# Kernel tuning notes

Hardware: AMD Instinct MI355X
Metric: run time of the kernel (lower is better)

## Reference

```python
import jax, jax.numpy as jnp
import numpy as np

B = 32768          # batch (replay-buffer minibatch)
OBS, ACT = 17, 6   # HalfCheetah-style dims
IN = OBS + ACT
H = 256            # hidden width hard-coded in the module
N = 10             # num_q_nets


def setup_inputs() -> dict:
    key = jax.random.key(0)
    ks = jax.random.split(key, 8)
    # PyTorch Linear default init: U(-1/sqrt(fan_in), 1/sqrt(fan_in)); scale randn similarly.
    s1, s2, s3 = 1.0 / np.sqrt(IN), 1.0 / np.sqrt(H), 1.0 / np.sqrt(H)
    return {
        "state": jax.random.normal(ks[0], (B, OBS), dtype=jnp.float32),
        "action": jax.random.uniform(ks[1], (B, ACT), dtype=jnp.float32, minval=-1.0, maxval=1.0),
        "W1": jax.random.normal(ks[2], (N, IN, H), dtype=jnp.float32) * s1,
        "b1": jax.random.normal(ks[3], (N, H), dtype=jnp.float32) * s1,
        "W2": jax.random.normal(ks[4], (N, H, H), dtype=jnp.float32) * s2,
        "b2": jax.random.normal(ks[5], (N, H), dtype=jnp.float32) * s2,
        "W3": jax.random.normal(ks[6], (N, H, 1), dtype=jnp.float32) * s3,
        "b3": jax.random.normal(ks[7], (N, 1), dtype=jnp.float32) * s3,
    }


def reference(state, action, W1, b1, W2, b2, W3, b3):
    # x: [B, OBS+ACT]
    x = jnp.concatenate([state, action], axis=1)
    # batched-over-ensemble GEMMs; n=ensemble member, b=batch
    h1 = jax.nn.relu(jnp.einsum("bi,nih->nbh", x, W1) + b1[:, None, :])   # [N,B,H]
    h2 = jax.nn.relu(jnp.einsum("nbh,nho->nbo", h1, W2) + b2[:, None, :])  # [N,B,H]
    out = jnp.einsum("nbh,nho->nbo", h2, W3) + b3[:, None, :]              # [N,B,1]
    return out
```

## Files before the change

### kernel.cpp

```cpp
#include <hip/hip_runtime.h>
#include <hip/hip_bf16.h>


typedef __attribute__((ext_vector_type(8))) short bf16x8;
typedef __attribute__((ext_vector_type(4))) float f32x4;

#define B_TOTAL 32768
#define NQ 10
#define HDIM 256
#define BT 128

#define XP_ELEMS  (B_TOTAL * 32)
#define W1P_ELEMS (NQ * 16 * 64 * 8)
#define W2P_ELEMS (NQ * 8 * 16 * 64 * 8)

__device__ __forceinline__ unsigned short f2bf(float f) {
  unsigned int u = __float_as_uint(f);
  u = u + 0x7FFFu + ((u >> 16) & 1u);
  return (unsigned short)(u >> 16);
}

__device__ __forceinline__ unsigned int pk2bf(float a, float b) {
  union { __hip_bfloat162 h; unsigned int u; } cv;
  cv.h = __float22bfloat162_rn(make_float2(a, b));
  return cv.u;
}

__global__ void pack_all_kernel(const float* __restrict__ state,
                                const float* __restrict__ action,
                                const float* __restrict__ W1,
                                const float* __restrict__ W2,
                                unsigned short* __restrict__ xp,
                                unsigned short* __restrict__ w1p,
                                unsigned short* __restrict__ w2p) {
  int t = blockIdx.x * 256 + threadIdx.x;
  const int NX  = B_TOTAL * 4;
  const int NW1 = NQ * 16 * 64;
  if (t < NX) {
    int b = t >> 2, seg = t & 3;
    unsigned short v[8];
    if (seg < 2) {
      const float* sp = state + (size_t)b * 17 + seg * 8;
#pragma unroll
      for (int j = 0; j < 8; j++) v[j] = f2bf(sp[j]);
    } else if (seg == 2) {
      v[0] = f2bf(state[(size_t)b * 17 + 16]);
#pragma unroll
      for (int j = 0; j < 6; j++) v[1 + j] = f2bf(action[(size_t)b * 6 + j]);
      v[7] = 0;
    } else {
#pragma unroll
      for (int j = 0; j < 8; j++) v[j] = 0;
    }
    *(uint4*)&xp[(size_t)t * 8] = *(const uint4*)v;
  } else if (t < NX + NW1) {
    int u = t - NX;
    int lane = u & 63, mt = (u >> 6) & 15, n = u >> 10;
    int m = lane & 15, q = lane >> 4;
    int outc = mt * 16 + m;
    unsigned short v[8];
#pragma unroll
    for (int j = 0; j < 8; j++) {
      int k = q * 8 + j;
      v[j] = (k < 23) ? f2bf(W1[(n * 23 + k) * 256 + outc]) : (unsigned short)0;
    }
    *(uint4*)&w1p[(size_t)u * 8] = *(const uint4*)v;
  } else {
    int u = t - NX - NW1;
    int lane = u & 63, mt = (u >> 6) & 15, kt = (u >> 10) & 7, n = u >> 13;
    int m = lane & 15, q = lane >> 4;
    int outc = mt * 16 + m;
    unsigned short v[8];
#pragma unroll
    for (int j = 0; j < 8; j++) {
      int h = kt * 32 + q * 8 + j;
      v[j] = f2bf(W2[((size_t)(n * 256 + h)) * 256 + outc]);
    }
    *(uint4*)&w2p[(size_t)u * 8] = *(const uint4*)v;
  }
}

__global__ __launch_bounds__(512, 4) void fused_ensemble_kernel(
    const unsigned short* __restrict__ xp,
    const unsigned short* __restrict__ w1p,
    const float* __restrict__ b1,
    const unsigned short* __restrict__ w2p,
    const float* __restrict__ b2,
    const float* __restrict__ W3,
    const float* __restrict__ b3,
    float* __restrict__ out) {
  __shared__ __align__(16) unsigned short hs[32 * BT * 8];
  __shared__ float red[8 * 64];

  const int tid = threadIdx.x;
  const int lane = tid & 63;
  const int w = tid >> 6;
  const int m = lane & 15;
  const int q = lane >> 4;
  const int cg = w >> 1;
  const int colg = w & 1;

  const int n = blockIdx.x >> 8;
  const int row0 = (blockIdx.x & 255) * BT;

  const unsigned short* w2n = w2p + (size_t)n * (8 * 16 * 64 * 8);

  f32x4 acc[4][4];
  {
    bf16x8 af[4], bfr[4];
#pragma unroll
    for (int nt = 0; nt < 4; nt++) {
      int col = row0 + colg * 64 + nt * 16 + m;
      bfr[nt] = *(const bf16x8*)(xp + (size_t)col * 32 + q * 8);
    }
#pragma unroll
    for (int mt = 0; mt < 4; mt++)
      af[mt] = *(const bf16x8*)(w1p + (((size_t)n * 16 + cg * 4 + mt) * 64 + lane) * 8);
#pragma unroll
    for (int mt = 0; mt < 4; mt++) {
      float4 bv = *(const float4*)&b1[n * HDIM + (cg * 4 + mt) * 16 + q * 4];
      f32x4 bi = (f32x4){bv.x, bv.y, bv.z, bv.w};
#pragma unroll
      for (int nt = 0; nt < 4; nt++) acc[mt][nt] = bi;
    }
#pragma unroll
    for (int nt = 0; nt < 4; nt++)
#pragma unroll
      for (int mt = 0; mt < 4; mt++)
        acc[mt][nt] = __builtin_amdgcn_mfma_f32_16x16x32_bf16(af[mt], bfr[nt], acc[mt][nt], 0, 0, 0);
  }

  bf16x8 aS[2][4];
  bf16x8 bS[2][4];
#pragma unroll
  for (int sl = 0; sl < 2; sl++)
#pragma unroll
    for (int mt = 0; mt < 4; mt++)
      aS[sl][mt] = *(const bf16x8*)(w2n + (((size_t)sl * 16 + cg * 4 + mt) * 64 + lane) * 8);

  f32x4 acc2[4][4];
#pragma unroll
  for (int mt = 0; mt < 4; mt++) {
    float4 bv = *(const float4*)&b2[n * HDIM + (cg * 4 + mt) * 16 + q * 4];
    f32x4 bi = (f32x4){bv.x, bv.y, bv.z, bv.w};
#pragma unroll
    for (int nt = 0; nt < 4; nt++) acc2[mt][nt] = bi;
  }

#pragma unroll
  for (int mt = 0; mt < 4; mt++) {
    int kq = cg * 8 + mt * 2 + (q >> 1);
    int joff = (q & 1) * 4;
#pragma unroll
    for (int nt = 0; nt < 4; nt++) {
      int col = colg * 64 + nt * 16 + m;
      f32x4 a = acc[mt][nt];
      uint2 wv;
      wv.x = pk2bf(fmaxf(a[0], 0.f), fmaxf(a[1], 0.f));
      wv.y = pk2bf(fmaxf(a[2], 0.f), fmaxf(a[3], 0.f));
      *(uint2*)&hs[((size_t)kq * BT + col) * 8 + joff] = wv;
    }
  }
  __syncthreads();

  {
#pragma unroll
    for (int sl = 0; sl < 2; sl++)
#pragma unroll
      for (int nt = 0; nt < 4; nt++)
        bS[sl][nt] = *(const bf16x8*)&hs[(((size_t)sl * 4 + q) * BT + colg * 64 + nt * 16 + m) * 8];

#pragma unroll
    for (int kt = 0; kt < 8; kt++) {
      const int sl = kt & 1;
#pragma unroll
      for (int nt = 0; nt < 4; nt++)
#pragma unroll
        for (int mt = 0; mt < 4; mt++)
          acc2[mt][nt] = __builtin_amdgcn_mfma_f32_16x16x32_bf16(
              aS[sl][mt], bS[sl][nt], acc2[mt][nt], 0, 0, 0);
      if (kt + 2 < 8) {
#pragma unroll
        for (int mt = 0; mt < 4; mt++)
          aS[sl][mt] = *(const bf16x8*)(w2n + (((size_t)(kt + 2) * 16 + cg * 4 + mt) * 64 + lane) * 8);
#pragma unroll
        for (int nt = 0; nt < 4; nt++)
          bS[sl][nt] = *(const bf16x8*)&hs[(((size_t)(kt + 2) * 4 + q) * BT + colg * 64 + nt * 16 + m) * 8];
      }
    }
  }

  {
    float4 w3v[4];
#pragma unroll
    for (int mt = 0; mt < 4; mt++)
      w3v[mt] = *(const float4*)&W3[n * HDIM + (cg * 4 + mt) * 16 + q * 4];
    float p[4];
#pragma unroll
    for (int nt = 0; nt < 4; nt++) {
      float s = 0.f;
#pragma unroll
      for (int mt = 0; mt < 4; mt++) {
        f32x4 a = acc2[mt][nt];
        float4 wv = w3v[mt];
        s = fmaf(fmaxf(a[0], 0.f), wv.x, s);
        s = fmaf(fmaxf(a[1], 0.f), wv.y, s);
        s = fmaf(fmaxf(a[2], 0.f), wv.z, s);
        s = fmaf(fmaxf(a[3], 0.f), wv.w, s);
      }
      s += __shfl_xor(s, 16, 64);
      s += __shfl_xor(s, 32, 64);
      p[nt] = s;
    }
    if (q == 0) {
#pragma unroll
      for (int nt = 0; nt < 4; nt++) red[w * 64 + nt * 16 + m] = p[nt];
    }
    __syncthreads();
    if (tid < BT) {
      int g = tid >> 6, lc = tid & 63;
      float s = b3[n];
#pragma unroll
      for (int c = 0; c < 4; c++) s += red[(c * 2 + g) * 64 + lc];
      out[(size_t)n * B_TOTAL + row0 + tid] = s;
    }
  }
}

extern "C" void kernel_launch(void* const* d_in, const int* in_sizes, int n_in,
                              void* d_out, int out_size, void* d_ws, size_t ws_size,
                              hipStream_t stream) {
  const float* state  = (const float*)d_in[0];
  const float* action = (const float*)d_in[1];
  const float* W1 = (const float*)d_in[2];
  const float* b1 = (const float*)d_in[3];
  const float* W2 = (const float*)d_in[4];
  const float* b2 = (const float*)d_in[5];
  const float* W3 = (const float*)d_in[6];
  const float* b3 = (const float*)d_in[7];
  float* out = (float*)d_out;

  unsigned short* xp  = (unsigned short*)d_ws;
  unsigned short* w1p = (unsigned short*)((char*)d_ws + (size_t)XP_ELEMS * 2);
  unsigned short* w2p = (unsigned short*)((char*)d_ws + (size_t)(XP_ELEMS + W1P_ELEMS) * 2);

  pack_all_kernel<<<872, 256, 0, stream>>>(state, action, W1, W2, xp, w1p, w2p);
  fused_ensemble_kernel<<<NQ * (B_TOTAL / BT), 512, 0, stream>>>(
      xp, w1p, b1, w2p, b2, W3, b3, out);
}
```

Measured before the change: 120.6 us.

## Replace block barrier with per-pair LDS flags and rotated K-loop order

The workgroup-wide barrier between layer-1 output staging and the layer-2 GEMM is replaced by per-column-group atomic counters in shared memory. Each wave first consumes the K-slices its own pair of waves produced, then the others in rotated order, spinning with s_sleep until the producing pair has signalled. This is meant to let waves start layer-2 MFMAs without waiting for the whole block. It adds an extra barrier at kernel start, spin-wait and atomic overhead, and changes how the W2 and hidden-state loads are prefetched.

```diff
diff --git a/kernel.cpp b/kernel.cpp
--- a/kernel.cpp
+++ b/kernel.cpp
@@ -91,6 +91,7 @@
     float* __restrict__ out) {
   __shared__ __align__(16) unsigned short hs[32 * BT * 8];
   __shared__ float red[8 * 64];
+  __shared__ int flg[4];
 
   const int tid = threadIdx.x;
   const int lane = tid & 63;
@@ -105,6 +106,9 @@
 
   const unsigned short* w2n = w2p + (size_t)n * (8 * 16 * 64 * 8);
 
+  if (tid < 4) flg[tid] = 0;
+  __syncthreads();
+
   f32x4 acc[4][4];
   {
     bf16x8 af[4], bfr[4];
@@ -130,13 +134,11 @@
         acc[mt][nt] = __builtin_amdgcn_mfma_f32_16x16x32_bf16(af[mt], bfr[nt], acc[mt][nt], 0, 0, 0);
   }
 
-  bf16x8 aS[2][4];
-  bf16x8 bS[2][4];
-#pragma unroll
-  for (int sl = 0; sl < 2; sl++)
-#pragma unroll
-    for (int mt = 0; mt < 4; mt++)
-      aS[sl][mt] = *(const bf16x8*)(w2n + (((size_t)sl * 16 + cg * 4 + mt) * 64 + lane) * 8);
+  bf16x8 aE[4];
+  const int kt0 = 2 * cg;
+#pragma unroll
+  for (int mt = 0; mt < 4; mt++)
+    aE[mt] = *(const bf16x8*)(w2n + (((size_t)kt0 * 16 + cg * 4 + mt) * 64 + lane) * 8);
 
   f32x4 acc2[4][4];
 #pragma unroll
@@ -161,32 +163,44 @@
       *(uint2*)&hs[((size_t)kq * BT + col) * 8 + joff] = wv;
     }
   }
-  __syncthreads();
+  __threadfence_block();
+  if (lane == 0)
+    __hip_atomic_fetch_add(&flg[cg], 1, __ATOMIC_RELEASE, __HIP_MEMORY_SCOPE_WORKGROUP);
 
   {
 #pragma unroll
-    for (int sl = 0; sl < 2; sl++)
-#pragma unroll
-      for (int nt = 0; nt < 4; nt++)
-        bS[sl][nt] = *(const bf16x8*)&hs[(((size_t)sl * 4 + q) * BT + colg * 64 + nt * 16 + m) * 8];
-
-#pragma unroll
-    for (int kt = 0; kt < 8; kt++) {
-      const int sl = kt & 1;
+    for (int ii = 0; ii < 4; ii++) {
+      const int ktE = (2 * cg + 2 * ii) & 7;
+      const int pair = ktE >> 1;
+      while (__hip_atomic_load(&flg[pair], __ATOMIC_ACQUIRE, __HIP_MEMORY_SCOPE_WORKGROUP) < 2) {
+        __builtin_amdgcn_s_sleep(1);
+      }
+      bf16x8 bE[4], bO[4], aO[4];
+#pragma unroll
+      for (int nt = 0; nt < 4; nt++)
+        bE[nt] = *(const bf16x8*)&hs[(((size_t)ktE * 4 + q) * BT + colg * 64 + nt * 16 + m) * 8];
+#pragma unroll
+      for (int nt = 0; nt < 4; nt++)
+        bO[nt] = *(const bf16x8*)&hs[(((size_t)(ktE + 1) * 4 + q) * BT + colg * 64 + nt * 16 + m) * 8];
+#pragma unroll
+      for (int mt = 0; mt < 4; mt++)
+        aO[mt] = *(const bf16x8*)(w2n + (((size_t)(ktE + 1) * 16 + cg * 4 + mt) * 64 + lane) * 8);
 #pragma unroll
       for (int nt = 0; nt < 4; nt++)
 #pragma unroll
         for (int mt = 0; mt < 4; mt++)
-          acc2[mt][nt] = __builtin_amdgcn_mfma_f32_16x16x32_bf16(
-              aS[sl][mt], bS[sl][nt], acc2[mt][nt], 0, 0, 0);
-      if (kt + 2 < 8) {
+          acc2[mt][nt] = __builtin_amdgcn_mfma_f32_16x16x32_bf16(aE[mt], bE[nt], acc2[mt][nt], 0, 0, 0);
+      if (ii < 3) {
+        const int ktN = (ktE + 2) & 7;
 #pragma unroll
         for (int mt = 0; mt < 4; mt++)
-          aS[sl][mt] = *(const bf16x8*)(w2n + (((size_t)(kt + 2) * 16 + cg * 4 + mt) * 64 + lane) * 8);
-#pragma unroll
-        for (int nt = 0; nt < 4; nt++)
-          bS[sl][nt] = *(const bf16x8*)&hs[(((size_t)(kt + 2) * 4 + q) * BT + colg * 64 + nt * 16 + m) * 8];
+          aE[mt] = *(const bf16x8*)(w2n + (((size_t)ktN * 16 + cg * 4 + mt) * 64 + lane) * 8);
       }
+#pragma unroll
+      for (int nt = 0; nt < 4; nt++)
+#pragma unroll
+        for (int mt = 0; mt < 4; mt++)
+          acc2[mt][nt] = __builtin_amdgcn_mfma_f32_16x16x32_bf16(aO[mt], bO[nt], acc2[mt][nt], 0, 0, 0);
     }
   }
 
```

Result: slower. 125.9 us (+4.3%).

## Make ensemble MLP kernel persistent with W2 slice held in registers

Applied to the files above, without the earlier changes.

Turns the fused kernel into a persistent one: the grid is 52 blocks per ensemble member, each with 4 waves, and each block loops over 64-row batch tiles. Each wave loads its W2 slice for all K steps into registers once and reuses it for every tile, so W2 is no longer re-streamed from cache for every 128-row block. In exchange, each wave needs many more registers, blocks are smaller, fewer waves are resident per CU to hide latency, and 512 tiles do not split evenly across 52 blocks.

```diff
diff --git a/kernel.cpp b/kernel.cpp
--- a/kernel.cpp
+++ b/kernel.cpp
@@ -8,7 +8,9 @@
 #define B_TOTAL 32768
 #define NQ 10
 #define HDIM 256
-#define BT 128
+#define BT 64
+#define TILES 512
+#define BPN 52
 
 #define XP_ELEMS  (B_TOTAL * 32)
 #define W1P_ELEMS (NQ * 16 * 64 * 8)
@@ -80,7 +82,7 @@
   }
 }
 
-__global__ __launch_bounds__(512, 4) void fused_ensemble_kernel(
+__global__ __launch_bounds__(256, 2) void fused_ensemble_kernel(
     const unsigned short* __restrict__ xp,
     const unsigned short* __restrict__ w1p,
     const float* __restrict__ b1,
@@ -90,139 +92,139 @@
     const float* __restrict__ b3,
     float* __restrict__ out) {
   __shared__ __align__(16) unsigned short hs[32 * BT * 8];
-  __shared__ float red[8 * 64];
+  __shared__ float red[4 * BT];
 
   const int tid = threadIdx.x;
   const int lane = tid & 63;
   const int w = tid >> 6;
   const int m = lane & 15;
   const int q = lane >> 4;
-  const int cg = w >> 1;
-  const int colg = w & 1;
-
-  const int n = blockIdx.x >> 8;
-  const int row0 = (blockIdx.x & 255) * BT;
+
+  const int n = blockIdx.x / BPN;
+  const int slot = blockIdx.x - n * BPN;
 
   const unsigned short* w2n = w2p + (size_t)n * (8 * 16 * 64 * 8);
 
-  f32x4 acc[4][4];
-  {
-    bf16x8 af[4], bfr[4];
-#pragma unroll
-    for (int nt = 0; nt < 4; nt++) {
-      int col = row0 + colg * 64 + nt * 16 + m;
-      bfr[nt] = *(const bf16x8*)(xp + (size_t)col * 32 + q * 8);
-    }
+  bf16x8 aW[8][4];
+#pragma unroll
+  for (int kt = 0; kt < 8; kt++)
 #pragma unroll
     for (int mt = 0; mt < 4; mt++)
-      af[mt] = *(const bf16x8*)(w1p + (((size_t)n * 16 + cg * 4 + mt) * 64 + lane) * 8);
+      aW[kt][mt] = *(const bf16x8*)(w2n + (((size_t)kt * 16 + w * 4 + mt) * 64 + lane) * 8);
+
+  const float b3n = b3[n];
+
+  for (int tile = slot; tile < TILES; tile += BPN) {
+    const int row0 = tile * BT;
+
+    f32x4 acc[4][4];
+    {
+      bf16x8 af[4], bfr[4];
+#pragma unroll
+      for (int nt = 0; nt < 4; nt++) {
+        int col = row0 + nt * 16 + m;
+        bfr[nt] = *(const bf16x8*)(xp + (size_t)col * 32 + q * 8);
+      }
+#pragma unroll
+      for (int mt = 0; mt < 4; mt++)
+        af[mt] = *(const bf16x8*)(w1p + (((size_t)n * 16 + w * 4 + mt) * 64 + lane) * 8);
+#pragma unroll
+      for (int mt = 0; mt < 4; mt++) {
+        float4 bv = *(const float4*)&b1[n * HDIM + (w * 4 + mt) * 16 + q * 4];
+        f32x4 bi = (f32x4){bv.x, bv.y, bv.z, bv.w};
+#pragma unroll
+        for (int nt = 0; nt < 4; nt++) acc[mt][nt] = bi;
+      }
+#pragma unroll
+      for (int nt = 0; nt < 4; nt++)
+#pragma unroll
+        for (int mt = 0; mt < 4; mt++)
+          acc[mt][nt] = __builtin_amdgcn_mfma_f32_16x16x32_bf16(af[mt], bfr[nt], acc[mt][nt], 0, 0, 0);
+    }
+
 #pragma unroll
     for (int mt = 0; mt < 4; mt++) {
-      float4 bv = *(const float4*)&b1[n * HDIM + (cg * 4 + mt) * 16 + q * 4];
+      int kq = w * 8 + mt * 2 + (q >> 1);
+      int joff = (q & 1) * 4;
+#pragma unroll
+      for (int nt = 0; nt < 4; nt++) {
+        int col = nt * 16 + m;
+        f32x4 a = acc[mt][nt];
+        uint2 wv;
+        wv.x = pk2bf(fmaxf(a[0], 0.f), fmaxf(a[1], 0.f));
+        wv.y = pk2bf(fmaxf(a[2], 0.f), fmaxf(a[3], 0.f));
+        *(uint2*)&hs[((size_t)kq * BT + col) * 8 + joff] = wv;
+      }
+    }
+
+    f32x4 acc2[4][4];
+#pragma unroll
+    for (int mt = 0; mt < 4; mt++) {
+      float4 bv = *(const float4*)&b2[n * HDIM + (w * 4 + mt) * 16 + q * 4];
       f32x4 bi = (f32x4){bv.x, bv.y, bv.z, bv.w};
 #pragma unroll
-      for (int nt = 0; nt < 4; nt++) acc[mt][nt] = bi;
-    }
-#pragma unroll
-    for (int nt = 0; nt < 4; nt++)
+      for (int nt = 0; nt < 4; nt++) acc2[mt][nt] = bi;
+    }
+    __syncthreads();
+
+    {
+      bf16x8 bS[2][4];
+#pragma unroll
+      for (int sl = 0; sl < 2; sl++)
+#pragma unroll
+        for (int nt = 0; nt < 4; nt++)
+          bS[sl][nt] = *(const bf16x8*)&hs[(((size_t)sl * 4 + q) * BT + nt * 16 + m) * 8];
+
+#pragma unroll
+      for (int kt = 0; kt < 8; kt++) {
+        const int sl = kt & 1;
+#pragma unroll
+        for (int nt = 0; nt < 4; nt++)
+#pragma unroll
+          for (int mt = 0; mt < 4; mt++)
+            acc2[mt][nt] = __builtin_amdgcn_mfma_f32_16x16x32_bf16(
+                aW[kt][mt], bS[sl][nt], acc2[mt][nt], 0, 0, 0);
+        if (kt + 2 < 8) {
+#pragma unroll
+          for (int nt = 0; nt < 4; nt++)
+            bS[sl][nt] = *(const bf16x8*)&hs[(((size_t)(kt + 2) * 4 + q) * BT + nt * 16 + m) * 8];
+        }
+      }
+    }
+
+    {
+      float4 w3v[4];
 #pragma unroll
       for (int mt = 0; mt < 4; mt++)
-        acc[mt][nt] = __builtin_amdgcn_mfma_f32_16x16x32_bf16(af[mt], bfr[nt], acc[mt][nt], 0, 0, 0);
-  }
-
-  bf16x8 aS[2][4];
-  bf16x8 bS[2][4];
-#pragma unroll
-  for (int sl = 0; sl < 2; sl++)
-#pragma unroll
-    for (int mt = 0; mt < 4; mt++)
-      aS[sl][mt] = *(const bf16x8*)(w2n + (((size_t)sl * 16 + cg * 4 + mt) * 64 + lane) * 8);
-
-  f32x4 acc2[4][4];
-#pragma unroll
-  for (int mt = 0; mt < 4; mt++) {
-    float4 bv = *(const float4*)&b2[n * HDIM + (cg * 4 + mt) * 16 + q * 4];
-    f32x4 bi = (f32x4){bv.x, bv.y, bv.z, bv.w};
-#pragma unroll
-    for (int nt = 0; nt < 4; nt++) acc2[mt][nt] = bi;
-  }
-
-#pragma unroll
-  for (int mt = 0; mt < 4; mt++) {
-    int kq = cg * 8 + mt * 2 + (q >> 1);
-    int joff = (q & 1) * 4;
-#pragma unroll
-    for (int nt = 0; nt < 4; nt++) {
-      int col = colg * 64 + nt * 16 + m;
-      f32x4 a = acc[mt][nt];
-      uint2 wv;
-      wv.x = pk2bf(fmaxf(a[0], 0.f), fmaxf(a[1], 0.f));
-      wv.y = pk2bf(fmaxf(a[2], 0.f), fmaxf(a[3], 0.f));
-      *(uint2*)&hs[((size_t)kq * BT + col) * 8 + joff] = wv;
-    }
-  }
-  __syncthreads();
-
-  {
-#pragma unroll
-    for (int sl = 0; sl < 2; sl++)
-#pragma unroll
-      for (int nt = 0; nt < 4; nt++)
-        bS[sl][nt] = *(const bf16x8*)&hs[(((size_t)sl * 4 + q) * BT + colg * 64 + nt * 16 + m) * 8];
-
-#pragma unroll
-    for (int kt = 0; kt < 8; kt++) {
-      const int sl = kt & 1;
-#pragma unroll
-      for (int nt = 0; nt < 4; nt++)
-#pragma unroll
-        for (int mt = 0; mt < 4; mt++)
-          acc2[mt][nt] = __builtin_amdgcn_mfma_f32_16x16x32_bf16(
-              aS[sl][mt], bS[sl][nt], acc2[mt][nt], 0, 0, 0);
-      if (kt + 2 < 8) {
-#pragma unroll
-        for (int mt = 0; mt < 4; mt++)
-          aS[sl][mt] = *(const bf16x8*)(w2n + (((size_t)(kt + 2) * 16 + cg * 4 + mt) * 64 + lane) * 8);
-#pragma unroll
-        for (int nt = 0; nt < 4; nt++)
-          bS[sl][nt] = *(const bf16x8*)&hs[(((size_t)(kt + 2) * 4 + q) * BT + colg * 64 + nt * 16 + m) * 8];
-      }
-    }
-  }
-
-  {
-    float4 w3v[4];
-#pragma unroll
-    for (int mt = 0; mt < 4; mt++)
-      w3v[mt] = *(const float4*)&W3[n * HDIM + (cg * 4 + mt) * 16 + q * 4];
-    float p[4];
-#pragma unroll
-    for (int nt = 0; nt < 4; nt++) {
-      float s = 0.f;
-#pragma unroll
-      for (int mt = 0; mt < 4; mt++) {
-        f32x4 a = acc2[mt][nt];
-        float4 wv = w3v[mt];
-        s = fmaf(fmaxf(a[0], 0.f), wv.x, s);
-        s = fmaf(fmaxf(a[1], 0.f), wv.y, s);
-        s = fmaf(fmaxf(a[2], 0.f), wv.z, s);
-        s = fmaf(fmaxf(a[3], 0.f), wv.w, s);
-      }
-      s += __shfl_xor(s, 16, 64);
-      s += __shfl_xor(s, 32, 64);
-      p[nt] = s;
-    }
-    if (q == 0) {
-#pragma unroll
-      for (int nt = 0; nt < 4; nt++) red[w * 64 + nt * 16 + m] = p[nt];
-    }
-    __syncthreads();
-    if (tid < BT) {
-      int g = tid >> 6, lc = tid & 63;
-      float s = b3[n];
-#pragma unroll
-      for (int c = 0; c < 4; c++) s += red[(c * 2 + g) * 64 + lc];
-      out[(size_t)n * B_TOTAL + row0 + tid] = s;
+        w3v[mt] = *(const float4*)&W3[n * HDIM + (w * 4 + mt) * 16 + q * 4];
+      float p[4];
+#pragma unroll
+      for (int nt = 0; nt < 4; nt++) {
+        float s = 0.f;
+#pragma unroll
+        for (int mt = 0; mt < 4; mt++) {
+          f32x4 a = acc2[mt][nt];
+          float4 wv = w3v[mt];
+          s = fmaf(fmaxf(a[0], 0.f), wv.x, s);
+          s = fmaf(fmaxf(a[1], 0.f), wv.y, s);
+          s = fmaf(fmaxf(a[2], 0.f), wv.z, s);
+          s = fmaf(fmaxf(a[3], 0.f), wv.w, s);
+        }
+        s += __shfl_xor(s, 16, 64);
+        s += __shfl_xor(s, 32, 64);
+        p[nt] = s;
+      }
+      if (q == 0) {
+#pragma unroll
+        for (int nt = 0; nt < 4; nt++) red[w * BT + nt * 16 + m] = p[nt];
+      }
+      __syncthreads();
+      if (tid < BT) {
+        float s = b3n;
+#pragma unroll
+        for (int c = 0; c < 4; c++) s += red[c * BT + tid];
+        out[(size_t)n * B_TOTAL + row0 + tid] = s;
+      }
     }
   }
 }
@@ -245,6 +247,6 @@
   unsigned short* w2p = (unsigned short*)((char*)d_ws + (size_t)(XP_ELEMS + W1P_ELEMS) * 2);
 
   pack_all_kernel<<<872, 256, 0, stream>>>(state, action, W1, W2, xp, w1p, w2p);
-  fused_ensemble_kernel<<<NQ * (B_TOTAL / BT), 512, 0, stream>>>(
+  fused_ensemble_kernel<<<NQ * BPN, 256, 0, stream>>>(
       xp, w1p, b1, w2p, b2, W3, b3, out);
 }
```

Measured after the change: 162.2 us. 34.4% more time.
